# Performance work log

Measured on AMD Instinct MI355X. Metric: run time of the kernel, lower is better.

Reference implementation:

```python
import jax, jax.numpy as jnp
import numpy as np

# ---- architecture constants (from init_kwargs / arch_args) ----
IN_BITS, IN_FRAC, BITS_PER_STREAM = 8, 4, 2
N_STREAMS = IN_BITS // BITS_PER_STREAM          # 4
W_BITS, BITS_PER_SLICE = 8, 2
N_SLICES = W_BITS // BITS_PER_SLICE             # 4
ADC_BITS = 5
ADC_MAX = 2.0 ** ADC_BITS - 1.0                 # 31
SUBARRAY_SIZE = 128
IC, OC, K, STRIDE, PAD = 64, 64, 3, 1, 1
F_TOTAL = IC * K * K                            # 576 unfolded features
N_SUB = (F_TOTAL + SUBARRAY_SIZE - 1) // SUBARRAY_SIZE  # 5 subarrays
CHUNK = -(-F_TOTAL // N_SUB)                    # 116, matches torch.chunk sizes


def bit_stream(x):
    """VectorizedInputBitStreaming.forward: fixed-point quantize + two's complement + bit-serial split."""
    int_bits = IN_BITS - IN_FRAC - 1
    max_val = 2.0 ** int_bits - 2.0 ** (-IN_FRAC)
    q = jnp.round(jnp.clip(x, -(2.0 ** int_bits), max_val) * (2 ** IN_FRAC)).astype(jnp.int32)
    q = jnp.where(q < 0, (1 << IN_BITS) + q, q)  # two's complement encode
    shifts = jnp.arange(0, IN_BITS, BITS_PER_STREAM, dtype=jnp.int32)
    return ((q[..., None] >> shifts) & ((1 << BITS_PER_STREAM) - 1)).astype(jnp.float32)


def bit_slice(w):
    """VectorizedWeightBitSlicing.forward: pos/neg split, normalize by max abs, integer bit-slice."""
    wp = jnp.maximum(w, 0.0)
    wn = jnp.maximum(-w, 0.0)
    max_abs = jnp.maximum(wp.max(), wn.max())
    max_abs = jnp.where(max_abs > 0, max_abs, 1.0)
    mv = 2 ** W_BITS - 1
    pi = jnp.round(wp / max_abs * mv).astype(jnp.int32)
    ni = jnp.round(wn / max_abs * mv).astype(jnp.int32)
    shifts = jnp.arange(0, W_BITS, BITS_PER_SLICE, dtype=jnp.int32)
    mask = (1 << BITS_PER_SLICE) - 1
    pos = ((pi[..., None] >> shifts) & mask).astype(jnp.float32)
    neg = ((ni[..., None] >> shifts) & mask).astype(jnp.float32)
    return pos, neg, max_abs


def adc(x):
    """Nbit_ADC simulated: uniform round + clip to [0, 2^adc_bits - 1]."""
    return jnp.clip(jnp.round(x), 0.0, ADC_MAX)


def _forward(inputs, weight):
    # unfold -> (B, IC*K*K, H', W') with (c, kh, kw)-major feature ordering like F.unfold
    patches = jax.lax.conv_general_dilated_patches(
        inputs, (K, K), (STRIDE, STRIDE), [(PAD, PAD), (PAD, PAD)])
    B, F, H, W = patches.shape
    P = H * W
    patches = patches.reshape(B, F, P)

    streams = bit_stream(patches)                     # (B, F, P, S)
    pos_sl, neg_sl, norm = bit_slice(weight)
    pos_m = pos_sl.reshape(OC, F, N_SLICES)           # (O, F, T)
    neg_m = neg_sl.reshape(OC, F, N_SLICES)

    # zero-pad feature dim to N_SUB*CHUNK and reshape into subarray chunks
    pad = N_SUB * CHUNK - F
    streams = jnp.pad(streams, ((0, 0), (0, pad), (0, 0), (0, 0))).reshape(B, N_SUB, CHUNK, P, N_STREAMS)
    pos_m = jnp.pad(pos_m, ((0, 0), (0, pad), (0, 0))).reshape(OC, N_SUB, CHUNK, N_SLICES)
    neg_m = jnp.pad(neg_m, ((0, 0), (0, pad), (0, 0))).reshape(OC, N_SUB, CHUNK, N_SLICES)

    # per-subarray analog MAC: (c, b, o, p, s, t)
    pos_r = jnp.einsum('bcfps,ocft->cbopst', streams, pos_m)
    neg_r = jnp.einsum('bcfps,ocft->cbopst', streams, neg_m)

    # ADC quantize, then weight by 2^(stream*bits) * 2^(slice*bits), sum over s,t and subarrays c
    scale = (2.0 ** (jnp.arange(N_STREAMS) * BITS_PER_STREAM))[:, None] * \
            (2.0 ** (jnp.arange(N_SLICES) * BITS_PER_SLICE))[None, :]
    diff = jnp.einsum('cbopst,st->bop', adc(pos_r) - adc(neg_r), scale)

    out = diff * norm / (2.0 ** IN_BITS - 1.0)
    return out.reshape(B, OC, H, W), jnp.float32(0.0)


def setup_inputs() -> dict:
    key = jax.random.key(0)
    k1, k2 = jax.random.split(key)
    inputs = jax.random.normal(k1, (4, IC, 32, 32), dtype=jnp.float32)
    # kaiming_normal_-like init
    weight = jax.random.normal(k2, (OC, IC, K, K), dtype=jnp.float32) * (2.0 / (IC * K * K)) ** 0.5
    return {"inputs": inputs, "weight": weight}


def reference(inputs, weight):
    return _forward(inputs, weight)
```

## Files before the change

kernel.cpp:

```cpp
#include <hip/hip_runtime.h>
#include <stdint.h>


typedef int v4i __attribute__((ext_vector_type(4)));
typedef unsigned int v4u __attribute__((ext_vector_type(4)));

#define WS_PART   0
#define WS_AQ     1024
#define N_PART    144

__device__ __forceinline__ unsigned char quant_in(float x) {
  x = fminf(fmaxf(x, -8.0f), 7.9375f);
  int q = (int)rintf(x * 16.0f);
  return (unsigned char)(q & 255);
}

__global__ __launch_bounds__(256) void k_prep(
    const float* __restrict__ in, const float* __restrict__ w,
    unsigned char* __restrict__ Aq, float* __restrict__ part,
    float* __restrict__ out_scalar)
{
  int bid = blockIdx.x, tid = threadIdx.x;
  if (bid == 0 && tid == 0) out_scalar[0] = 0.0f;
  if (bid < 2560) {
    unsigned int widx = bid * 256 + tid;
    unsigned int m  = ((widx >> 5) * 52429u) >> 18;
    unsigned int kw = widx - m * 160;
    int b = m >> 10, p = m & 1023;
    int y = p >> 5, x = p & 31;
    unsigned int pack = 0;
    #pragma unroll
    for (int i = 0; i < 4; ++i) {
      unsigned int k = kw * 4 + i;
      unsigned int c = k >> 7;
      unsigned int j = k & 127;
      unsigned int csize = (c == 4) ? 112 : 116;
      unsigned int bv = 0;
      if (j < csize) {
        unsigned int f  = c * 116 + j;
        unsigned int ic = (f * 7282u) >> 16;
        unsigned int r9 = f - ic * 9;
        unsigned int dy = (r9 * 11u) >> 5;
        unsigned int dx = r9 - dy * 3;
        int iy = y + (int)dy - 1, ix = x + (int)dx - 1;
        if (iy >= 0 && iy < 32 && ix >= 0 && ix < 32)
          bv = quant_in(in[((b * 64 + ic) * 32 + iy) * 32 + ix]);
      }
      pack |= bv << (8 * i);
    }
    ((unsigned int*)Aq)[widx] = pack;
  } else {
    int t = (bid - 2560) * 256 + tid;
    const float4 wv = ((const float4*)w)[t];
    float a = fmaxf(fmaxf(fabsf(wv.x), fabsf(wv.y)),
                    fmaxf(fabsf(wv.z), fabsf(wv.w)));
    #pragma unroll
    for (int off = 32; off > 0; off >>= 1)
      a = fmaxf(a, __shfl_down(a, off, 64));
    if ((tid & 63) == 0)
      part[(bid - 2560) * 4 + (tid >> 6)] = a;
  }
}

__device__ __forceinline__ v4i bits2(v4u w, int s) {
  v4u r = (w >> (unsigned)(2 * s)) & 0x03030303u;
  return (v4i)r;
}

#define BROW 656

__global__ __launch_bounds__(256) void k_main(
    const unsigned char* __restrict__ Aq, const float* __restrict__ w,
    const float* __restrict__ part, float* __restrict__ out)
{
  __shared__ unsigned char Bl[2][16][BROW];
  __shared__ float s_norm;

  int tid   = threadIdx.x;
  int lane  = tid & 63;
  int wave  = tid >> 6;
  int mtile = blockIdx.x >> 2;
  int otile = blockIdx.x & 3;

  #pragma unroll
  for (int i = 0; i < 21; ++i) {
    int d = i * 256 + tid;
    if (d < 2 * 16 * BROW / 4) ((unsigned int*)Bl)[d] = 0u;
  }
  if (wave == 0) {
    float a = part[lane];
    a = fmaxf(a, part[lane + 64]);
    if (lane < 16) a = fmaxf(a, part[lane + 128]);
    #pragma unroll
    for (int off = 32; off > 0; off >>= 1)
      a = fmaxf(a, __shfl_down(a, off, 64));
    if (lane == 0) s_norm = (a > 0.0f) ? a : 1.0f;
  }
  __syncthreads();

  float norm = s_norm;
  float sc = 255.0f / norm;
  #pragma unroll
  for (int it = 0; it < 36; ++it) {
    int idx = it * 256 + tid;
    unsigned int ol = (((unsigned)idx >> 6) * 7282u) >> 16;
    unsigned int f  = idx - ol * 576;
    float wv = w[(otile * 16 + ol) * 576 + f];
    unsigned int c = (f * 565u) >> 16;
    unsigned int j = f - c * 116;
    int kpos = c * 128 + j;
    Bl[0][ol][kpos] = (unsigned char)(int)rintf(fmaxf(wv, 0.0f) * sc);
    Bl[1][ol][kpos] = (unsigned char)(int)rintf(fmaxf(-wv, 0.0f) * sc);
  }
  __syncthreads();

  int r16  = lane & 15;
  int kgrp = lane >> 4;
  int m = mtile * 64 + wave * 16 + r16;
  const unsigned char* ap = Aq + m * 640 + kgrp * 16;
  const unsigned char* bp = &Bl[0][r16][kgrp * 16];
  const unsigned char* bn = &Bl[1][r16][kgrp * 16];

  v4i outacc = {0, 0, 0, 0};

  #pragma unroll
  for (int c = 0; c < 5; ++c) {
    v4u a0 = *(const v4u*)(ap + c * 128);
    v4u a1 = *(const v4u*)(ap + c * 128 + 64);
    v4u p0 = *(const v4u*)(bp + c * 128);
    v4u p1 = *(const v4u*)(bp + c * 128 + 64);
    v4u n0 = *(const v4u*)(bn + c * 128);
    v4u n1 = *(const v4u*)(bn + c * 128 + 64);

    v4i btp0[4], btp1[4], btn0[4], btn1[4];
    #pragma unroll
    for (int t = 0; t < 4; ++t) {
      btp0[t] = bits2(p0, t); btp1[t] = bits2(p1, t);
      btn0[t] = bits2(n0, t); btn1[t] = bits2(n1, t);
    }

    #pragma unroll
    for (int s = 0; s < 4; ++s) {
      v4i as0 = bits2(a0, s), as1 = bits2(a1, s);
      #pragma unroll
      for (int t = 0; t < 4; ++t) {
        v4i z = {0, 0, 0, 0};
        v4i pacc = __builtin_amdgcn_mfma_i32_16x16x64_i8(as0, btp0[t], z, 0, 0, 0);
        pacc     = __builtin_amdgcn_mfma_i32_16x16x64_i8(as1, btp1[t], pacc, 0, 0, 0);
        v4i nacc = __builtin_amdgcn_mfma_i32_16x16x64_i8(as0, btn0[t], z, 0, 0, 0);
        nacc     = __builtin_amdgcn_mfma_i32_16x16x64_i8(as1, btn1[t], nacc, 0, 0, 0);
        int sh = 2 * (s + t);
        #pragma unroll
        for (int r = 0; r < 4; ++r) {
          int d = (pacc[r] < 31 ? pacc[r] : 31) - (nacc[r] < 31 ? nacc[r] : 31);
          outacc[r] += d << sh;
        }
      }
    }
  }

  float fsc = norm / 255.0f;
  int oc = otile * 16 + r16;
  #pragma unroll
  for (int r = 0; r < 4; ++r) {
    int mo = mtile * 64 + wave * 16 + kgrp * 4 + r;
    int b = mo >> 10, p = mo & 1023;
    out[(b * 64 + oc) * 1024 + p] = (float)outacc[r] * fsc;
  }
}

extern "C" void kernel_launch(void* const* d_in, const int* in_sizes, int n_in,
                              void* d_out, int out_size, void* d_ws, size_t ws_size,
                              hipStream_t stream) {
  const float* inp = (const float*)d_in[0];
  const float* wgt = (const float*)d_in[1];
  float* out = (float*)d_out;
  unsigned char* ws = (unsigned char*)d_ws;

  float*         part = (float*)(ws + WS_PART);
  unsigned char* Aq   = ws + WS_AQ;

  k_prep<<<2596, 256, 0, stream>>>(inp, wgt, Aq, part, out + 262144);
  k_main<<<256, 256, 0, stream>>>(Aq, wgt, part, out);
}
```

Before: 78.28 us.

## Precompute bit-sliced weight planes in prep kernel and read them from global

Weight quantization and 2-bit slicing move out of the main kernel into four extra prep blocks. Each of those blocks redundantly computes the global max-abs norm, then writes eight pre-sliced byte planes (pos/neg × 4 slices) plus zeroed padding to the workspace. The main kernel drops its LDS staging, the two barriers and the per-block re-quantization of weights, and loads B fragments directly from global/L2. In exchange it issues more global loads per block (8 planes instead of 2), and the prep blocks each reread the full weight tensor.

Result: slower. 88.96 us (+13.6%).

```diff
diff --git a/kernel.cpp b/kernel.cpp
--- a/kernel.cpp
+++ b/kernel.cpp
@@ -5,9 +5,10 @@
 typedef int v4i __attribute__((ext_vector_type(4)));
 typedef unsigned int v4u __attribute__((ext_vector_type(4)));
 
-#define WS_PART   0
-#define WS_AQ     1024
-#define N_PART    144
+#define WS_NORM   0
+#define WS_B      1024
+#define WS_AQ     331776
+#define B_PLANE   40960
 
 __device__ __forceinline__ unsigned char quant_in(float x) {
   x = fminf(fmaxf(x, -8.0f), 7.9375f);
@@ -17,12 +18,13 @@
 
 __global__ __launch_bounds__(256) void k_prep(
     const float* __restrict__ in, const float* __restrict__ w,
-    unsigned char* __restrict__ Aq, float* __restrict__ part,
-    float* __restrict__ out_scalar)
+    unsigned char* __restrict__ Aq, unsigned char* __restrict__ Bq,
+    float* __restrict__ nrm, float* __restrict__ out_scalar)
 {
+  __shared__ float smax[4];
   int bid = blockIdx.x, tid = threadIdx.x;
-  if (bid == 0 && tid == 0) out_scalar[0] = 0.0f;
   if (bid < 2560) {
+    if (bid == 0 && tid == 0) out_scalar[0] = 0.0f;
     unsigned int widx = bid * 256 + tid;
     unsigned int m  = ((widx >> 5) * 52429u) >> 18;
     unsigned int kw = widx - m * 160;
@@ -50,15 +52,66 @@
     }
     ((unsigned int*)Aq)[widx] = pack;
   } else {
-    int t = (bid - 2560) * 256 + tid;
-    const float4 wv = ((const float4*)w)[t];
-    float a = fmaxf(fmaxf(fabsf(wv.x), fabsf(wv.y)),
-                    fmaxf(fabsf(wv.z), fabsf(wv.w)));
+    int q = bid - 2560;
+    float a = 0.0f;
+    #pragma unroll 4
+    for (int i = 0; i < 36; ++i) {
+      float4 v = ((const float4*)w)[i * 256 + tid];
+      a = fmaxf(a, fmaxf(fmaxf(fabsf(v.x), fabsf(v.y)),
+                         fmaxf(fabsf(v.z), fabsf(v.w))));
+    }
     #pragma unroll
     for (int off = 32; off > 0; off >>= 1)
       a = fmaxf(a, __shfl_down(a, off, 64));
-    if ((tid & 63) == 0)
-      part[(bid - 2560) * 4 + (tid >> 6)] = a;
+    if ((tid & 63) == 0) smax[tid >> 6] = a;
+    __syncthreads();
+    float norm = fmaxf(fmaxf(smax[0], smax[1]), fmaxf(smax[2], smax[3]));
+    norm = (norm > 0.0f) ? norm : 1.0f;
+    if (q == 0 && tid == 0) nrm[0] = norm;
+    float sc = 255.0f / norm;
+
+    unsigned int* Bd = (unsigned int*)Bq;
+    for (int g = 0; g < 9; ++g) {
+      int grp = g * 1024 + q * 256 + tid;
+      unsigned int m4 = (unsigned)grp >> 4;
+      unsigned int oc = (m4 * 7282u) >> 16;
+      unsigned int fg = (unsigned)grp - oc * 144;
+      unsigned int f  = fg * 4;
+      unsigned int c  = (f * 565u) >> 16;
+      unsigned int j  = f - c * 116;
+      unsigned int col = c * 32 + (j >> 2);
+      float4 wv = ((const float4*)w)[grp];
+      int p0 = (int)rintf(fmaxf(wv.x, 0.0f) * sc);
+      int p1 = (int)rintf(fmaxf(wv.y, 0.0f) * sc);
+      int p2 = (int)rintf(fmaxf(wv.z, 0.0f) * sc);
+      int p3 = (int)rintf(fmaxf(wv.w, 0.0f) * sc);
+      int n0 = (int)rintf(fmaxf(-wv.x, 0.0f) * sc);
+      int n1 = (int)rintf(fmaxf(-wv.y, 0.0f) * sc);
+      int n2 = (int)rintf(fmaxf(-wv.z, 0.0f) * sc);
+      int n3 = (int)rintf(fmaxf(-wv.w, 0.0f) * sc);
+      unsigned int Pp = (unsigned)p0 | ((unsigned)p1 << 8) |
+                        ((unsigned)p2 << 16) | ((unsigned)p3 << 24);
+      unsigned int Pn = (unsigned)n0 | ((unsigned)n1 << 8) |
+                        ((unsigned)n2 << 16) | ((unsigned)n3 << 24);
+      #pragma unroll
+      for (int t = 0; t < 4; ++t) {
+        Bd[((t)     * 64 + oc) * 160 + col] = (Pp >> (2 * t)) & 0x03030303u;
+        Bd[((4 + t) * 64 + oc) * 160 + col] = (Pn >> (2 * t)) & 0x03030303u;
+      }
+    }
+    int gtid = q * 256 + tid;
+    #pragma unroll
+    for (int e = 0; e < 8; ++e) {
+      int idx = gtid * 8 + e;
+      int plane = idx >> 10;
+      int r = idx & 1023;
+      int oc = r >> 4;
+      int s = r & 15;
+      int c, d;
+      if (s < 12) { c = (s * 11) >> 5; d = 29 + s - 3 * c; }
+      else        { c = 4;             d = s + 16; }
+      Bd[(plane * 64 + oc) * 160 + c * 32 + d] = 0u;
+    }
   }
 }
 
@@ -67,59 +120,22 @@
   return (v4i)r;
 }
 
-#define BROW 656
-
 __global__ __launch_bounds__(256) void k_main(
-    const unsigned char* __restrict__ Aq, const float* __restrict__ w,
-    const float* __restrict__ part, float* __restrict__ out)
+    const unsigned char* __restrict__ Aq, const unsigned char* __restrict__ Bq,
+    const float* __restrict__ nrm, float* __restrict__ out)
 {
-  __shared__ unsigned char Bl[2][16][BROW];
-  __shared__ float s_norm;
-
   int tid   = threadIdx.x;
   int lane  = tid & 63;
   int wave  = tid >> 6;
   int mtile = blockIdx.x >> 2;
   int otile = blockIdx.x & 3;
 
-  #pragma unroll
-  for (int i = 0; i < 21; ++i) {
-    int d = i * 256 + tid;
-    if (d < 2 * 16 * BROW / 4) ((unsigned int*)Bl)[d] = 0u;
-  }
-  if (wave == 0) {
-    float a = part[lane];
-    a = fmaxf(a, part[lane + 64]);
-    if (lane < 16) a = fmaxf(a, part[lane + 128]);
-    #pragma unroll
-    for (int off = 32; off > 0; off >>= 1)
-      a = fmaxf(a, __shfl_down(a, off, 64));
-    if (lane == 0) s_norm = (a > 0.0f) ? a : 1.0f;
-  }
-  __syncthreads();
-
-  float norm = s_norm;
-  float sc = 255.0f / norm;
-  #pragma unroll
-  for (int it = 0; it < 36; ++it) {
-    int idx = it * 256 + tid;
-    unsigned int ol = (((unsigned)idx >> 6) * 7282u) >> 16;
-    unsigned int f  = idx - ol * 576;
-    float wv = w[(otile * 16 + ol) * 576 + f];
-    unsigned int c = (f * 565u) >> 16;
-    unsigned int j = f - c * 116;
-    int kpos = c * 128 + j;
-    Bl[0][ol][kpos] = (unsigned char)(int)rintf(fmaxf(wv, 0.0f) * sc);
-    Bl[1][ol][kpos] = (unsigned char)(int)rintf(fmaxf(-wv, 0.0f) * sc);
-  }
-  __syncthreads();
-
   int r16  = lane & 15;
   int kgrp = lane >> 4;
   int m = mtile * 64 + wave * 16 + r16;
   const unsigned char* ap = Aq + m * 640 + kgrp * 16;
-  const unsigned char* bp = &Bl[0][r16][kgrp * 16];
-  const unsigned char* bn = &Bl[1][r16][kgrp * 16];
+  const unsigned char* bp = Bq + (otile * 16 + r16) * 640 + kgrp * 16;
+  float fsc = nrm[0] / 255.0f;
 
   v4i outacc = {0, 0, 0, 0};
 
@@ -127,16 +143,11 @@
   for (int c = 0; c < 5; ++c) {
     v4u a0 = *(const v4u*)(ap + c * 128);
     v4u a1 = *(const v4u*)(ap + c * 128 + 64);
-    v4u p0 = *(const v4u*)(bp + c * 128);
-    v4u p1 = *(const v4u*)(bp + c * 128 + 64);
-    v4u n0 = *(const v4u*)(bn + c * 128);
-    v4u n1 = *(const v4u*)(bn + c * 128 + 64);
-
-    v4i btp0[4], btp1[4], btn0[4], btn1[4];
+    v4i b0[8], b1[8];
     #pragma unroll
-    for (int t = 0; t < 4; ++t) {
-      btp0[t] = bits2(p0, t); btp1[t] = bits2(p1, t);
-      btn0[t] = bits2(n0, t); btn1[t] = bits2(n1, t);
+    for (int pl = 0; pl < 8; ++pl) {
+      b0[pl] = *(const v4i*)(bp + pl * B_PLANE + c * 128);
+      b1[pl] = *(const v4i*)(bp + pl * B_PLANE + c * 128 + 64);
     }
 
     #pragma unroll
@@ -145,10 +156,10 @@
       #pragma unroll
       for (int t = 0; t < 4; ++t) {
         v4i z = {0, 0, 0, 0};
-        v4i pacc = __builtin_amdgcn_mfma_i32_16x16x64_i8(as0, btp0[t], z, 0, 0, 0);
-        pacc     = __builtin_amdgcn_mfma_i32_16x16x64_i8(as1, btp1[t], pacc, 0, 0, 0);
-        v4i nacc = __builtin_amdgcn_mfma_i32_16x16x64_i8(as0, btn0[t], z, 0, 0, 0);
-        nacc     = __builtin_amdgcn_mfma_i32_16x16x64_i8(as1, btn1[t], nacc, 0, 0, 0);
+        v4i pacc = __builtin_amdgcn_mfma_i32_16x16x64_i8(as0, b0[t], z, 0, 0, 0);
+        pacc     = __builtin_amdgcn_mfma_i32_16x16x64_i8(as1, b1[t], pacc, 0, 0, 0);
+        v4i nacc = __builtin_amdgcn_mfma_i32_16x16x64_i8(as0, b0[4 + t], z, 0, 0, 0);
+        nacc     = __builtin_amdgcn_mfma_i32_16x16x64_i8(as1, b1[4 + t], nacc, 0, 0, 0);
         int sh = 2 * (s + t);
         #pragma unroll
         for (int r = 0; r < 4; ++r) {
@@ -159,7 +170,6 @@
     }
   }
 
-  float fsc = norm / 255.0f;
   int oc = otile * 16 + r16;
   #pragma unroll
   for (int r = 0; r < 4; ++r) {
@@ -177,9 +187,10 @@
   float* out = (float*)d_out;
   unsigned char* ws = (unsigned char*)d_ws;
 
-  float*         part = (float*)(ws + WS_PART);
-  unsigned char* Aq   = ws + WS_AQ;
+  float*         nrm = (float*)(ws + WS_NORM);
+  unsigned char* Bq  = ws + WS_B;
+  unsigned char* Aq  = ws + WS_AQ;
 
-  k_prep<<<2596, 256, 0, stream>>>(inp, wgt, Aq, part, out + 262144);
-  k_main<<<256, 256, 0, stream>>>(Aq, wgt, part, out);
+  k_prep<<<2564, 256, 0, stream>>>(inp, wgt, Aq, Bq, nrm, out + 262144);
+  k_main<<<256, 256, 0, stream>>>(Aq, Bq, nrm, out);
 }
```
